# Kernel tuning notes

Hardware: AMD Instinct MI355X
Metric: run time of the kernel (lower is better)

## Reference

```python
import jax, jax.numpy as jnp
import numpy as np
import math

N_EMBD = 1024
N_HEAD = 16
D_FF = 4 * N_EMBD
B, T = 4, 2048

def gelu_tanh(x):
    return 0.5 * x * (1.0 + jnp.tanh(jnp.sqrt(2.0 / jnp.pi).astype(x.dtype) * (x + 0.044715 * x ** 3)))

def layernorm(x, g, b, eps=1e-5):
    mu = jnp.mean(x, axis=-1, keepdims=True)
    var = jnp.var(x, axis=-1, keepdims=True)
    return (x - mu) * jax.lax.rsqrt(var + eps) * g + b

def setup_inputs() -> dict:
    key = jax.random.key(0)
    ks = jax.random.split(key, 12)
    s = lambda fan_in: 1.0 / np.sqrt(fan_in)
    return {
        "x": jax.random.normal(ks[0], (B, T, N_EMBD), jnp.float32),
        "ln1_g": jnp.ones((N_EMBD,), jnp.float32),
        "ln1_b": jnp.zeros((N_EMBD,), jnp.float32),
        "w_attn": jax.random.normal(ks[1], (N_EMBD, 3 * N_EMBD), jnp.float32) * s(N_EMBD),
        "b_attn": jnp.zeros((3 * N_EMBD,), jnp.float32),
        "w_proj": jax.random.normal(ks[2], (N_EMBD, N_EMBD), jnp.float32) * s(N_EMBD),
        "b_proj": jnp.zeros((N_EMBD,), jnp.float32),
        "ln2_g": jnp.ones((N_EMBD,), jnp.float32),
        "ln2_b": jnp.zeros((N_EMBD,), jnp.float32),
        "w_fc": jax.random.normal(ks[3], (N_EMBD, D_FF), jnp.float32) * s(N_EMBD),
        "b_fc": jnp.zeros((D_FF,), jnp.float32),
        "w_fc2": jax.random.normal(ks[4], (D_FF, N_EMBD), jnp.float32) * s(D_FF),
        "b_fc2": jnp.zeros((N_EMBD,), jnp.float32),
    }

def reference(x, ln1_g, ln1_b, w_attn, b_attn, w_proj, b_proj,
              ln2_g, ln2_b, w_fc, b_fc, w_fc2, b_fc2):
    Bn, Tn, C = x.shape
    hs = C // N_HEAD
    # --- attention ---
    h = layernorm(x, ln1_g, ln1_b)
    qkv = h @ w_attn + b_attn  # [B,T,3C]
    q, k, v = jnp.split(qkv, 3, axis=-1)
    q = q.reshape(Bn, Tn, N_HEAD, hs).transpose(0, 2, 1, 3)
    k = k.reshape(Bn, Tn, N_HEAD, hs).transpose(0, 2, 1, 3)
    v = v.reshape(Bn, Tn, N_HEAD, hs).transpose(0, 2, 1, 3)
    att = jnp.einsum('bhqd,bhkd->bhqk', q, k) * (hs ** -0.5)
    mask = jnp.tril(jnp.ones((Tn, Tn), bool))
    att = jnp.where(mask, att, -jnp.inf)
    att = jax.nn.softmax(att, axis=-1)
    y = jnp.einsum('bhqk,bhkd->bhqd', att, v)
    y = y.transpose(0, 2, 1, 3).reshape(Bn, Tn, C)
    x = x + (y @ w_proj + b_proj)
    # --- MLP ---
    h2 = layernorm(x, ln2_g, ln2_b)
    h2 = gelu_tanh(h2 @ w_fc + b_fc)
    x = x + (h2 @ w_fc2 + b_fc2)
    return x
```

## Files before the change

kernel.cpp:

```cpp
#include <hip/hip_runtime.h>
#include <hip/hip_bf16.h>

#define B_ 4
#define T_ 2048
#define C_ 1024
#define NH_ 16
#define FF_ 4096
#define NT_ (B_*T_)

typedef short bf16x8 __attribute__((ext_vector_type(8)));
typedef float f32x4 __attribute__((ext_vector_type(4)));

#define LDS_AS(p) ((__attribute__((address_space(3))) uint32_t*)(p))
#define GLB_AS(p) ((const __attribute__((address_space(1))) uint32_t*)(p))

__device__ __forceinline__ float bf2f(__hip_bfloat16 v){ return __bfloat162float(v); }
__device__ __forceinline__ __hip_bfloat16 f2bf(float f){ return __float2bfloat16(f); }

__device__ __forceinline__ f32x4 mfma16(bf16x8 a, bf16x8 b, f32x4 c){
  return __builtin_amdgcn_mfma_f32_16x16x32_bf16(a, b, c, 0, 0, 0);
}

__global__ __launch_bounds__(256) void transpose_bf16(const float* __restrict__ in,
                                                      __hip_bfloat16* __restrict__ out,
                                                      int K, int N) {
  __shared__ float tile[32][33];
  const int n0 = blockIdx.x * 32, k0 = blockIdx.y * 32;
  const int x = threadIdx.x & 31, y = threadIdx.x >> 5;
  #pragma unroll
  for (int i = 0; i < 4; i++)
    tile[y + 8*i][x] = in[(size_t)(k0 + y + 8*i) * N + n0 + x];
  __syncthreads();
  #pragma unroll
  for (int i = 0; i < 4; i++)
    out[(size_t)(n0 + y + 8*i) * K + k0 + x] = f2bf(tile[x][y + 8*i]);
}

__global__ __launch_bounds__(256) void ln_bf16(const float* __restrict__ x,
                                               const float* __restrict__ g,
                                               const float* __restrict__ b,
                                               __hip_bfloat16* __restrict__ out) {
  const int row = blockIdx.x;
  const int tid = threadIdx.x;
  float4 v = ((const float4*)(x + (size_t)row * C_))[tid];
  float s  = v.x + v.y + v.z + v.w;
  float s2 = v.x*v.x + v.y*v.y + v.z*v.z + v.w*v.w;
  #pragma unroll
  for (int off = 32; off > 0; off >>= 1) {
    s  += __shfl_down(s,  off, 64);
    s2 += __shfl_down(s2, off, 64);
  }
  __shared__ float red[8];
  const int w = tid >> 6, l = tid & 63;
  if (l == 0) { red[w] = s; red[4 + w] = s2; }
  __syncthreads();
  s  = red[0] + red[1] + red[2] + red[3];
  s2 = red[4] + red[5] + red[6] + red[7];
  const float mu   = s * (1.0f / C_);
  const float var  = s2 * (1.0f / C_) - mu * mu;
  const float rstd = rsqrtf(var + 1e-5f);
  float4 gv = ((const float4*)g)[tid];
  float4 bv = ((const float4*)b)[tid];
  ushort4 o;
  __hip_bfloat16 t;
  t = f2bf((v.x - mu) * rstd * gv.x + bv.x); o.x = *(unsigned short*)&t;
  t = f2bf((v.y - mu) * rstd * gv.y + bv.y); o.y = *(unsigned short*)&t;
  t = f2bf((v.z - mu) * rstd * gv.z + bv.z); o.z = *(unsigned short*)&t;
  t = f2bf((v.w - mu) * rstd * gv.w + bv.w); o.w = *(unsigned short*)&t;
  ((ushort4*)out)[(size_t)row * (C_/4) + tid] = o;
}

template <int MODE>
__global__ __launch_bounds__(512, 1) void gemm256(const __hip_bfloat16* __restrict__ A,
                                                  const __hip_bfloat16* __restrict__ BT,
                                                  const float* __restrict__ bias,
                                                  const float* __restrict__ resid,
                                                  void* __restrict__ outp,
                                                  void* __restrict__ outp2,
                                                  int N, int K, int CW) {
  __shared__ __hip_bfloat16 Als[3][128 * 64];
  __shared__ __hip_bfloat16 Bls[3][256 * 64];
  const int tid = threadIdx.x;
  const int w = tid >> 6, l = tid & 63;
  const int wm = w >> 2, wn = w & 3;
  const int m_ = l & 15, q_ = l >> 4;
  const int lrow8 = l >> 3;
  const int gchunk = (l & 7) ^ lrow8;

  const int nbx = N >> 8;
  const int bid = blockIdx.x;
  const int x8 = bid & 7, i8 = bid >> 3;
  const int ccols = nbx / CW;
  const int RH = (int)(gridDim.x >> 3) / CW;
  const int tile_n = ((x8 % ccols) * CW + (i8 % CW)) << 8;
  const int tile_m = ((x8 / ccols) * RH + (i8 / CW)) << 7;

  f32x4 acc[4][4] = {};

#define STAGE3(buf_, k0_) do {                                                     \
    _Pragma("unroll")                                                              \
    for (int j = 0; j < 2; j++) {                                                  \
      const int rg = w*16 + j*8;                                                   \
      __builtin_amdgcn_global_load_lds(                                            \
        GLB_AS(A + (size_t)(tile_m + rg + lrow8) * K + (k0_) + gchunk*8),          \
        LDS_AS(&Als[buf_][rg*64]), 16, 0, 0);                                      \
    }                                                                              \
    _Pragma("unroll")                                                              \
    for (int j = 0; j < 4; j++) {                                                  \
      const int rg = w*32 + j*8;                                                   \
      __builtin_amdgcn_global_load_lds(                                            \
        GLB_AS(BT + (size_t)(tile_n + rg + lrow8) * K + (k0_) + gchunk*8),         \
        LDS_AS(&Bls[buf_][rg*64]), 16, 0, 0);                                      \
    }                                                                              \
  } while (0)

  const int nt = K >> 6;
  STAGE3(0, 0);
  STAGE3(1, 64);

  int cur = 0;
  #pragma unroll 1
  for (int t = 0; t < nt; t++) {
    const int nxt2 = (cur + 2 >= 3) ? cur - 1 : cur + 2;
    if (t + 2 < nt) {
      STAGE3(nxt2, (t + 2) * 64);
      asm volatile("s_waitcnt vmcnt(12)" ::: "memory");
    } else if (t + 1 < nt) {
      asm volatile("s_waitcnt vmcnt(6)" ::: "memory");
    } else {
      asm volatile("s_waitcnt vmcnt(0)" ::: "memory");
    }
    __builtin_amdgcn_s_barrier();

    bf16x8 bfr[2][4];
    #pragma unroll
    for (int kc = 0; kc < 2; kc++)
      #pragma unroll
      for (int ni = 0; ni < 4; ni++) {
        const int row = wn*64 + ni*16 + m_;
        bfr[kc][ni] = *(const bf16x8*)&Bls[cur][row*64 + (((kc*4 + q_) ^ (row & 7)) * 8)];
      }
    __builtin_amdgcn_s_setprio(1);
    #pragma unroll
    for (int mi = 0; mi < 4; mi++) {
      const int row = wm*64 + mi*16 + m_;
      const bf16x8 a0 = *(const bf16x8*)&Als[cur][row*64 + ((q_       ^ (row & 7)) * 8)];
      const bf16x8 a1 = *(const bf16x8*)&Als[cur][row*64 + (((4 + q_) ^ (row & 7)) * 8)];
      #pragma unroll
      for (int ni = 0; ni < 4; ni++) acc[mi][ni] = mfma16(a0, bfr[0][ni], acc[mi][ni]);
      #pragma unroll
      for (int ni = 0; ni < 4; ni++) acc[mi][ni] = mfma16(a1, bfr[1][ni], acc[mi][ni]);
    }
    __builtin_amdgcn_s_setprio(0);
    __builtin_amdgcn_s_barrier();
    cur = (cur + 1 >= 3) ? 0 : cur + 1;
  }
#undef STAGE3

  const int r0 = tile_m + wm * 64 + q_ * 4;
  const int c0 = tile_n + wn * 64 + m_;
  #pragma unroll
  for (int mi = 0; mi < 4; mi++) {
    #pragma unroll
    for (int r = 0; r < 4; r++) {
      const int row = r0 + mi * 16 + r;
      #pragma unroll
      for (int ni = 0; ni < 4; ni++) {
        const int col = c0 + ni * 16;
        float v = acc[mi][ni][r] + bias[col];
        if (MODE == 0) {
          if (tile_n < 2 * C_) {
            ((__hip_bfloat16*)outp)[(size_t)row * (2*C_) + col] = f2bf(v);
          } else {
            const int dg = col - 2 * C_;
            ((__hip_bfloat16*)outp2)[((size_t)((row >> 11) * 1024 + dg)) * T_ + (row & 2047)] = f2bf(v);
          }
        } else if (MODE == 1 || MODE == 3) {
          ((float*)outp)[(size_t)row * N + col] = resid[(size_t)row * N + col] + v;
        } else {
          const float u = 0.7978845608028654f * (v + 0.044715f * v * v * v);
          const float e = __expf(2.0f * u);
          ((__hip_bfloat16*)outp)[(size_t)row * N + col] = f2bf(v * (1.0f - 1.0f / (e + 1.0f)));
        }
      }
    }
  }
}

__global__ __launch_bounds__(256, 4) void flash_attn(const __hip_bfloat16* __restrict__ qk,
                                                     const __hip_bfloat16* __restrict__ vT,
                                                     __hip_bfloat16* __restrict__ y) {
  const int id  = blockIdx.x;
  const int xcd = id & 7;
  const int jj  = id >> 3;
  const int bh  = xcd * 8 + (jj >> 4);
  const int p   = jj & 15;
  const int b   = bh >> 4, h = bh & 15;
  const int tid = threadIdx.x, w = tid >> 6, l = tid & 63;
  const int m_ = l & 15, q_ = l >> 4;
  const int lrow8 = l >> 3;
  const int gchunk = (l & 7) ^ lrow8;

  __shared__ __hip_bfloat16 Kls[2][64 * 64];
  __shared__ __hip_bfloat16 Vls[64 * 64];
  __shared__ __hip_bfloat16 Pls[64 * 76];

  const size_t kgbase = (size_t)b * T_ * (2*C_) + C_ + h*64;
  const size_t vgbase = (size_t)bh * 64 * T_;

#define STAGE_K(kt_, buf_) do {                                                        \
    _Pragma("unroll")                                                                  \
    for (int j2 = 0; j2 < 2; j2++) {                                                   \
      const int rg = j2*32 + w*8;                                                      \
      __builtin_amdgcn_global_load_lds(                                                \
        GLB_AS(qk + kgbase + (size_t)((kt_)*64 + rg + lrow8)*(2*C_) + gchunk*8),       \
        LDS_AS(&Kls[buf_][rg*64]), 16, 0, 0);                                          \
    }                                                                                  \
  } while (0)

#define STAGE_V(kt_) do {                                                              \
    _Pragma("unroll")                                                                  \
    for (int j2 = 0; j2 < 2; j2++) {                                                   \
      const int rg = j2*32 + w*8;                                                      \
      __builtin_amdgcn_global_load_lds(                                                \
        GLB_AS(vT + vgbase + (size_t)(rg + lrow8)*T_ + (kt_)*64 + gchunk*8),           \
        LDS_AS(&Vls[rg*64]), 16, 0, 0);                                                \
    }                                                                                  \
  } while (0)

  #pragma unroll 1
  for (int ui = 0; ui < 2; ui++) {
    const int qt = ui ? (31 - p) : p;
    const int q0 = qt * 64;

    bf16x8 aq[2];
    {
      const float qscale = 0.125f * 1.44269504088896f;
      const size_t qbase = ((size_t)b * T_ + q0 + w*16 + m_) * (2*C_) + h*64;
      #pragma unroll
      for (int kh = 0; kh < 2; kh++) {
        union { uint4 u; __hip_bfloat16 h8[8]; } t;
        t.u = *(const uint4*)&qk[qbase + kh*32 + q_*8];
        __hip_bfloat16 a[8];
        #pragma unroll
        for (int jx = 0; jx < 8; jx++) a[jx] = f2bf(bf2f(t.h8[jx]) * qscale);
        aq[kh] = *(const bf16x8*)a;
      }
    }

    f32x4 accO[4] = {};
    float lsum[4] = {0.f, 0.f, 0.f, 0.f};

    STAGE_K(0, 0);
    asm volatile("s_waitcnt vmcnt(0)" ::: "memory");
    __builtin_amdgcn_s_barrier();

    int cur = 0;
    #pragma unroll 1
    for (int kt = 0; kt <= qt; kt++) {
      STAGE_V(kt);

      f32x4 s[4];
      #pragma unroll
      for (int ni = 0; ni < 4; ni++) {
        const int row = ni*16 + m_;
        const bf16x8 bk0 = *(const bf16x8*)&Kls[cur][row*64 + ((q_     ^ (row & 7)) * 8)];
        const bf16x8 bk1 = *(const bf16x8*)&Kls[cur][row*64 + (((4+q_) ^ (row & 7)) * 8)];
        f32x4 z = {};
        z = mfma16(aq[0], bk0, z);
        s[ni] = mfma16(aq[1], bk1, z);
      }

      if (kt < qt) STAGE_K(kt + 1, cur ^ 1);

      if (kt == qt) {
        const int qrow = w*16 + q_*4;
        #pragma unroll
        for (int ni = 0; ni < 4; ni++) {
          const int kcol = ni*16 + m_;
          #pragma unroll
          for (int r = 0; r < 4; r++)
            if (kcol > qrow + r) s[ni][r] = -1e30f;
        }
      }

      #pragma unroll
      for (int ni = 0; ni < 4; ni++)
        #pragma unroll
        for (int r = 0; r < 4; r++)
          s[ni][r] = exp2f(s[ni][r]);
      #pragma unroll
      for (int r = 0; r < 4; r++)
        lsum[r] += (s[0][r] + s[1][r]) + (s[2][r] + s[3][r]);
      #pragma unroll
      for (int ni = 0; ni < 4; ni++)
        #pragma unroll
        for (int r = 0; r < 4; r++)
          Pls[(w*16 + q_*4 + r) * 76 + ni*16 + m_] = f2bf(s[ni][r]);

      bf16x8 ap[2];
      ap[0] = *(const bf16x8*)&Pls[(w*16 + m_) * 76 + q_*8];
      ap[1] = *(const bf16x8*)&Pls[(w*16 + m_) * 76 + 32 + q_*8];

      if (kt < qt) asm volatile("s_waitcnt vmcnt(2)" ::: "memory");
      else         asm volatile("s_waitcnt vmcnt(0)" ::: "memory");
      __builtin_amdgcn_s_barrier();

      #pragma unroll
      for (int ni = 0; ni < 4; ni++) {
        const int row = ni*16 + m_;
        const bf16x8 bv0 = *(const bf16x8*)&Vls[row*64 + ((q_     ^ (row & 7)) * 8)];
        const bf16x8 bv1 = *(const bf16x8*)&Vls[row*64 + (((4+q_) ^ (row & 7)) * 8)];
        accO[ni] = mfma16(ap[0], bv0, accO[ni]);
        accO[ni] = mfma16(ap[1], bv1, accO[ni]);
      }

      asm volatile("s_waitcnt vmcnt(0) lgkmcnt(0)" ::: "memory");
      __builtin_amdgcn_s_barrier();
      cur ^= 1;
    }

    #pragma unroll
    for (int r = 0; r < 4; r++) {
      #pragma unroll
      for (int d = 1; d < 16; d <<= 1)
        lsum[r] += __shfl_xor(lsum[r], d, 64);
    }

    const size_t ybase = ((size_t)b * T_ + q0) * C_ + h*64;
    #pragma unroll
    for (int r = 0; r < 4; r++) {
      const int row = w*16 + q_*4 + r;
      const float linv = 1.0f / lsum[r];
      #pragma unroll
      for (int ni = 0; ni < 4; ni++)
        y[ybase + (size_t)row * C_ + ni*16 + m_] = f2bf(accO[ni][r] * linv);
    }
  }
#undef STAGE_K
#undef STAGE_V
}

extern "C" void kernel_launch(void* const* d_in, const int* in_sizes, int n_in,
                              void* d_out, int out_size, void* d_ws, size_t ws_size,
                              hipStream_t stream) {
  const float* x      = (const float*)d_in[0];
  const float* ln1_g  = (const float*)d_in[1];
  const float* ln1_b  = (const float*)d_in[2];
  const float* w_attn = (const float*)d_in[3];
  const float* b_attn = (const float*)d_in[4];
  const float* w_proj = (const float*)d_in[5];
  const float* b_proj = (const float*)d_in[6];
  const float* ln2_g  = (const float*)d_in[7];
  const float* ln2_b  = (const float*)d_in[8];
  const float* w_fc   = (const float*)d_in[9];
  const float* b_fc   = (const float*)d_in[10];
  const float* w_fc2  = (const float*)d_in[11];
  const float* b_fc2  = (const float*)d_in[12];
  float* out = (float*)d_out;

  char* ws = (char*)d_ws;
  const size_t MB = 1024 * 1024;
  __hip_bfloat16* h      = (__hip_bfloat16*)(ws);
  __hip_bfloat16* qk     = (__hip_bfloat16*)(ws + 16*MB);
  __hip_bfloat16* vT     = (__hip_bfloat16*)(ws + 48*MB);
  __hip_bfloat16* y      = (__hip_bfloat16*)(ws + 64*MB);
  float*          x2     = (float*)        (ws + 80*MB);
  __hip_bfloat16* h2     = (__hip_bfloat16*)(ws + 64*MB);
  __hip_bfloat16* gbuf   = (__hip_bfloat16*)(ws);
  __hip_bfloat16* wattnT = (__hip_bfloat16*)(ws + 112*MB);
  __hip_bfloat16* wprojT = (__hip_bfloat16*)(ws + 118*MB);
  __hip_bfloat16* wfcT   = (__hip_bfloat16*)(ws + 120*MB);
  __hip_bfloat16* wfc2T  = (__hip_bfloat16*)(ws + 128*MB);

  transpose_bf16<<<dim3(3*C_/32, C_/32), 256, 0, stream>>>(w_attn, wattnT, C_, 3*C_);
  transpose_bf16<<<dim3(C_/32,  C_/32), 256, 0, stream>>>(w_proj, wprojT, C_, C_);
  transpose_bf16<<<dim3(FF_/32, C_/32), 256, 0, stream>>>(w_fc,   wfcT,   C_, FF_);
  transpose_bf16<<<dim3(C_/32, FF_/32), 256, 0, stream>>>(w_fc2,  wfc2T,  FF_, C_);

  ln_bf16<<<NT_, 256, 0, stream>>>(x, ln1_g, ln1_b, h);
  gemm256<0><<<dim3(768), 512, 0, stream>>>(h, wattnT, b_attn, nullptr, qk, vT, 3*C_, C_, 6);
  flash_attn<<<dim3(1024), 256, 0, stream>>>(qk, vT, y);
  gemm256<1><<<dim3(256), 512, 0, stream>>>(y, wprojT, b_proj, x, x2, nullptr, C_, C_, 4);
  ln_bf16<<<NT_, 256, 0, stream>>>(x2, ln2_g, ln2_b, h2);
  gemm256<2><<<dim3(1024), 512, 0, stream>>>(h2, wfcT, b_fc, nullptr, gbuf, nullptr, FF_, C_, 4);
  gemm256<3><<<dim3(256), 512, 0, stream>>>(gbuf, wfc2T, b_fc2, x2, out, nullptr, C_, FF_, 4);
}
```

Before: 554.6 us.

## Enlarge GEMM tiles to 256x256 with double-buffered LDS and phased MFMA

Replaces the 128x256 triple-buffered GEMM with a 256x256 tile, double-buffered kernel. Each wave now owns 128x64 outputs, and LDS reads go through inline ds_read_b128 with precomputed swizzled addresses. The MFMA loop is split into four phases separated by barriers, and the grid sizes and the column-width swizzle for the FC2 GEMM are adjusted to match. The larger tile raises data reuse per LDS byte and per global load, at the cost of fewer blocks (128 for the N=1024 GEMMs, which leaves CUs idle on a 256-CU part), more accumulator registers, and more frequent barriers.

```diff
diff --git a/kernel.cpp b/kernel.cpp
--- a/kernel.cpp
+++ b/kernel.cpp
@@ -20,6 +20,9 @@
 __device__ __forceinline__ f32x4 mfma16(bf16x8 a, bf16x8 b, f32x4 c){
   return __builtin_amdgcn_mfma_f32_16x16x32_bf16(a, b, c, 0, 0, 0);
 }
+
+#define DSR(dst_, addr_, off_) \
+  asm volatile("ds_read_b128 %0, %1 offset:" #off_ : "=v"(dst_) : "v"(addr_))
 
 __global__ __launch_bounds__(256) void transpose_bf16(const float* __restrict__ in,
                                                       __hip_bfloat16* __restrict__ out,
@@ -71,96 +74,119 @@
 }
 
 template <int MODE>
-__global__ __launch_bounds__(512, 1) void gemm256(const __hip_bfloat16* __restrict__ A,
-                                                  const __hip_bfloat16* __restrict__ BT,
-                                                  const float* __restrict__ bias,
-                                                  const float* __restrict__ resid,
-                                                  void* __restrict__ outp,
-                                                  void* __restrict__ outp2,
-                                                  int N, int K, int CW) {
-  __shared__ __hip_bfloat16 Als[3][128 * 64];
-  __shared__ __hip_bfloat16 Bls[3][256 * 64];
+__global__ __launch_bounds__(512, 1) void gemm8p(const __hip_bfloat16* __restrict__ A,
+                                                 const __hip_bfloat16* __restrict__ BT,
+                                                 const float* __restrict__ bias,
+                                                 const float* __restrict__ resid,
+                                                 void* __restrict__ outp,
+                                                 void* __restrict__ outp2,
+                                                 int N, int K, int CW) {
+  __shared__ __hip_bfloat16 Als[2][256 * 64];
+  __shared__ __hip_bfloat16 Bls[2][256 * 64];
   const int tid = threadIdx.x;
   const int w = tid >> 6, l = tid & 63;
   const int wm = w >> 2, wn = w & 3;
   const int m_ = l & 15, q_ = l >> 4;
-  const int lrow8 = l >> 3;
-  const int gchunk = (l & 7) ^ lrow8;
+  const int w8 = w << 3;
+  const int srow = tid >> 3;
+  const int schunk = (tid & 7) ^ (srow & 7);
 
   const int nbx = N >> 8;
   const int bid = blockIdx.x;
   const int x8 = bid & 7, i8 = bid >> 3;
   const int ccols = nbx / CW;
-  const int RH = (int)(gridDim.x >> 3) / CW;
-  const int tile_n = ((x8 % ccols) * CW + (i8 % CW)) << 8;
-  const int tile_m = ((x8 / ccols) * RH + (i8 / CW)) << 7;
-
-  f32x4 acc[4][4] = {};
-
-#define STAGE3(buf_, k0_) do {                                                     \
-    _Pragma("unroll")                                                              \
-    for (int j = 0; j < 2; j++) {                                                  \
-      const int rg = w*16 + j*8;                                                   \
-      __builtin_amdgcn_global_load_lds(                                            \
-        GLB_AS(A + (size_t)(tile_m + rg + lrow8) * K + (k0_) + gchunk*8),          \
-        LDS_AS(&Als[buf_][rg*64]), 16, 0, 0);                                      \
-    }                                                                              \
-    _Pragma("unroll")                                                              \
-    for (int j = 0; j < 4; j++) {                                                  \
-      const int rg = w*32 + j*8;                                                   \
-      __builtin_amdgcn_global_load_lds(                                            \
-        GLB_AS(BT + (size_t)(tile_n + rg + lrow8) * K + (k0_) + gchunk*8),         \
-        LDS_AS(&Bls[buf_][rg*64]), 16, 0, 0);                                      \
-    }                                                                              \
+  const int RH = ((int)(gridDim.x >> 3)) / CW;
+  const int tile_n = ((x8 % ccols) * CW + i8 % CW) << 8;
+  const int tile_m = ((x8 / ccols) * RH + i8 / CW) << 8;
+
+  f32x4 acc[8][4] = {};
+
+  const __hip_bfloat16* gpa[4];
+  const __hip_bfloat16* gpb[4];
+  #pragma unroll
+  for (int i = 0; i < 4; i++) {
+    gpa[i] = A  + (size_t)(tile_m + i*64 + srow) * K + schunk*8;
+    gpb[i] = BT + (size_t)(tile_n + i*64 + srow) * K + schunk*8;
+  }
+
+#define STAGE_T(buf_) do {                                                        \
+    _Pragma("unroll")                                                             \
+    for (int i = 0; i < 4; i++) {                                                 \
+      __builtin_amdgcn_global_load_lds(GLB_AS(gpa[i]),                            \
+          LDS_AS(&Als[buf_][(i*64 + w8) * 64]), 16, 0, 0);                        \
+      gpa[i] += 64;                                                               \
+      __builtin_amdgcn_global_load_lds(GLB_AS(gpb[i]),                            \
+          LDS_AS(&Bls[buf_][(i*64 + w8) * 64]), 16, 0, 0);                        \
+      gpb[i] += 64;                                                               \
+    }                                                                             \
   } while (0)
 
+  const uint32_t ab = (uint32_t)(uintptr_t)LDS_AS(&Als[0][0]);
+  const uint32_t bb = (uint32_t)(uintptr_t)LDS_AS(&Bls[0][0]);
+  const uint32_t s0 = (uint32_t)(((q_)     ^ (m_ & 7)) * 16);
+  const uint32_t s1 = (uint32_t)(((4 + q_) ^ (m_ & 7)) * 16);
+  const uint32_t a_rd0 = ab + (uint32_t)((wm*128 + m_) * 128) + s0;
+  const uint32_t a_rd1 = ab + (uint32_t)((wm*128 + m_) * 128) + s1;
+  const uint32_t b_rd0 = bb + (uint32_t)((wn*64  + m_) * 128) + s0;
+  const uint32_t b_rd1 = bb + (uint32_t)((wn*64  + m_) * 128) + s1;
+
+#define PHASE(AOFF0, AOFF1, MI0, MI1) do {                                        \
+    bf16x8 a00, a01, a10, a11;                                                    \
+    DSR(a00, aa0, AOFF0); DSR(a01, aa1, AOFF0);                                   \
+    DSR(a10, aa0, AOFF1); DSR(a11, aa1, AOFF1);                                   \
+    asm volatile("s_waitcnt lgkmcnt(0)" ::: "memory");                            \
+    __builtin_amdgcn_sched_barrier(0);                                            \
+    __builtin_amdgcn_s_setprio(1);                                                \
+    _Pragma("unroll")                                                             \
+    for (int ni = 0; ni < 4; ni++) {                                              \
+      acc[MI0][ni] = mfma16(a00, bfr[0][ni], acc[MI0][ni]);                       \
+      acc[MI0][ni] = mfma16(a01, bfr[1][ni], acc[MI0][ni]);                       \
+      acc[MI1][ni] = mfma16(a10, bfr[0][ni], acc[MI1][ni]);                       \
+      acc[MI1][ni] = mfma16(a11, bfr[1][ni], acc[MI1][ni]);                       \
+    }                                                                             \
+    __builtin_amdgcn_s_setprio(0);                                                \
+    __builtin_amdgcn_s_barrier();                                                 \
+  } while (0)
+
+#define KTILE(CL) do {                                                            \
+    const uint32_t aa0 = a_rd0 + (CL)*32768u, aa1 = a_rd1 + (CL)*32768u;          \
+    const uint32_t bb0 = b_rd0 + (CL)*32768u, bb1 = b_rd1 + (CL)*32768u;          \
+    bf16x8 bfr[2][4];                                                             \
+    DSR(bfr[0][0], bb0, 0);    DSR(bfr[0][1], bb0, 2048);                         \
+    DSR(bfr[0][2], bb0, 4096); DSR(bfr[0][3], bb0, 6144);                         \
+    DSR(bfr[1][0], bb1, 0);    DSR(bfr[1][1], bb1, 2048);                         \
+    DSR(bfr[1][2], bb1, 4096); DSR(bfr[1][3], bb1, 6144);                         \
+    PHASE(0,     2048,  0, 1);                                                    \
+    PHASE(4096,  6144,  2, 3);                                                    \
+    PHASE(8192,  10240, 4, 5);                                                    \
+    PHASE(12288, 14336, 6, 7);                                                    \
+  } while (0)
+
   const int nt = K >> 6;
-  STAGE3(0, 0);
-  STAGE3(1, 64);
-
-  int cur = 0;
+  STAGE_T(0);
   #pragma unroll 1
-  for (int t = 0; t < nt; t++) {
-    const int nxt2 = (cur + 2 >= 3) ? cur - 1 : cur + 2;
+  for (int t = 0; t < nt; t += 2) {
+    STAGE_T(1);
+    asm volatile("s_waitcnt vmcnt(8)" ::: "memory");
+    __builtin_amdgcn_s_barrier();
+    KTILE(0);
     if (t + 2 < nt) {
-      STAGE3(nxt2, (t + 2) * 64);
-      asm volatile("s_waitcnt vmcnt(12)" ::: "memory");
-    } else if (t + 1 < nt) {
-      asm volatile("s_waitcnt vmcnt(6)" ::: "memory");
+      STAGE_T(0);
+      asm volatile("s_waitcnt vmcnt(8)" ::: "memory");
     } else {
       asm volatile("s_waitcnt vmcnt(0)" ::: "memory");
     }
     __builtin_amdgcn_s_barrier();
-
-    bf16x8 bfr[2][4];
-    #pragma unroll
-    for (int kc = 0; kc < 2; kc++)
-      #pragma unroll
-      for (int ni = 0; ni < 4; ni++) {
-        const int row = wn*64 + ni*16 + m_;
-        bfr[kc][ni] = *(const bf16x8*)&Bls[cur][row*64 + (((kc*4 + q_) ^ (row & 7)) * 8)];
-      }
-    __builtin_amdgcn_s_setprio(1);
-    #pragma unroll
-    for (int mi = 0; mi < 4; mi++) {
-      const int row = wm*64 + mi*16 + m_;
-      const bf16x8 a0 = *(const bf16x8*)&Als[cur][row*64 + ((q_       ^ (row & 7)) * 8)];
-      const bf16x8 a1 = *(const bf16x8*)&Als[cur][row*64 + (((4 + q_) ^ (row & 7)) * 8)];
-      #pragma unroll
-      for (int ni = 0; ni < 4; ni++) acc[mi][ni] = mfma16(a0, bfr[0][ni], acc[mi][ni]);
-      #pragma unroll
-      for (int ni = 0; ni < 4; ni++) acc[mi][ni] = mfma16(a1, bfr[1][ni], acc[mi][ni]);
-    }
-    __builtin_amdgcn_s_setprio(0);
-    __builtin_amdgcn_s_barrier();
-    cur = (cur + 1 >= 3) ? 0 : cur + 1;
+    KTILE(1);
   }
-#undef STAGE3
-
-  const int r0 = tile_m + wm * 64 + q_ * 4;
+#undef STAGE_T
+#undef PHASE
+#undef KTILE
+
+  const int r0 = tile_m + wm * 128 + q_ * 4;
   const int c0 = tile_n + wn * 64 + m_;
   #pragma unroll
-  for (int mi = 0; mi < 4; mi++) {
+  for (int mi = 0; mi < 8; mi++) {
     #pragma unroll
     for (int r = 0; r < 4; r++) {
       const int row = r0 + mi * 16 + r;
@@ -379,10 +405,10 @@
   transpose_bf16<<<dim3(C_/32, FF_/32), 256, 0, stream>>>(w_fc2,  wfc2T,  FF_, C_);
 
   ln_bf16<<<NT_, 256, 0, stream>>>(x, ln1_g, ln1_b, h);
-  gemm256<0><<<dim3(768), 512, 0, stream>>>(h, wattnT, b_attn, nullptr, qk, vT, 3*C_, C_, 6);
+  gemm8p<0><<<dim3(384), 512, 0, stream>>>(h, wattnT, b_attn, nullptr, qk, vT, 3*C_, C_, 6);
   flash_attn<<<dim3(1024), 256, 0, stream>>>(qk, vT, y);
-  gemm256<1><<<dim3(256), 512, 0, stream>>>(y, wprojT, b_proj, x, x2, nullptr, C_, C_, 4);
+  gemm8p<1><<<dim3(128), 512, 0, stream>>>(y, wprojT, b_proj, x, x2, nullptr, C_, C_, 4);
   ln_bf16<<<NT_, 256, 0, stream>>>(x2, ln2_g, ln2_b, h2);
-  gemm256<2><<<dim3(1024), 512, 0, stream>>>(h2, wfcT, b_fc, nullptr, gbuf, nullptr, FF_, C_, 4);
-  gemm256<3><<<dim3(256), 512, 0, stream>>>(gbuf, wfc2T, b_fc2, x2, out, nullptr, C_, FF_, 4);
-}
+  gemm8p<2><<<dim3(512), 512, 0, stream>>>(h2, wfcT, b_fc, nullptr, gbuf, nullptr, FF_, C_, 4);
+  gemm8p<3><<<dim3(128), 512, 0, stream>>>(gbuf, wfc2T, b_fc2, x2, out, nullptr, C_, FF_, 1);
+}
```

After: 583.6 us. 1.05x slower.
